# Kernel tuning notes

Measured on AMD Instinct MI355X. Metric: run time of the kernel, lower is better.

The kernel has to match this reference:

```python
import jax, jax.numpy as jnp
import numpy as np

N_NODES, N_EDGES, N_FEAT = 50000, 500000, 128
HID, LAT, N_GRAPHS = 256, 64, 512
HEADS, DH = 8, 32  # GAT: 8 heads x 32 = 256
EPS = 1e-5


def _seg_softmax(logits, seg, num):
    m = jax.ops.segment_max(logits, seg, num_segments=num)
    m = jnp.where(jnp.isfinite(m), m, 0.0)
    e = jnp.exp(logits - m[seg])
    s = jax.ops.segment_sum(e, seg, num_segments=num)
    return e / jnp.maximum(s[seg], 1e-16)


def _bn(h, g, b):  # BatchNorm1d, batch statistics
    mu = h.mean(0)
    var = h.var(0)
    return (h - mu) * jax.lax.rsqrt(var + EPS) * g + b


def _ln(h, g, b):
    mu = h.mean(-1, keepdims=True)
    var = h.var(-1, keepdims=True)
    return (h - mu) * jax.lax.rsqrt(var + EPS) * g + b


def setup_inputs() -> dict:
    key = jax.random.key(0)
    ks = iter(jax.random.split(key, 40))
    f = lambda *s: jax.random.normal(next(ks), s, dtype=jnp.float32) * 0.05
    inp = {
        'x': jax.random.normal(next(ks), (N_NODES, N_FEAT), dtype=jnp.float32),
        'W_emb': f(N_FEAT, HID), 'b_emb': f(HID),
        'W_gcn': f(HID, HID), 'b_gcn': f(HID),
        'W_gat': f(HID, HID), 'a_src': f(HEADS, DH), 'a_dst': f(HEADS, DH), 'b_gat': f(HID),
        'W_l': f(HID, HID), 'b_l': f(HID), 'W_r': f(HID, HID),
        'bn_gamma': jnp.ones((3, HID), jnp.float32), 'bn_beta': jnp.zeros((3, HID), jnp.float32),
        'Wg1': f(HID, HID // 2), 'bg1': f(HID // 2), 'Wg2': f(HID // 2, 1), 'bg2': f(1),
        'Wm1': f(HID, HID), 'bm1': f(HID), 'ln_m_g': jnp.ones(HID, jnp.float32), 'ln_m_b': jnp.zeros(HID, jnp.float32),
        'Wm2': f(HID, LAT), 'bm2': f(LAT),
        'Wv1': f(HID, HID), 'bv1': f(HID), 'ln_v_g': jnp.ones(HID, jnp.float32), 'ln_v_b': jnp.zeros(HID, jnp.float32),
        'Wv2': f(HID, LAT), 'bv2': f(LAT),
        'edge_index': jax.random.randint(next(ks), (2, N_EDGES), 0, N_NODES, dtype=jnp.int64),
        'batch': jnp.sort(jax.random.randint(next(ks), (N_NODES,), 0, N_GRAPHS, dtype=jnp.int64)),
    }
    return inp


def _forward(x, W_emb, b_emb, W_gcn, b_gcn, W_gat, a_src, a_dst, b_gat,
             W_l, b_l, W_r, bn_gamma, bn_beta, Wg1, bg1, Wg2, bg2,
             Wm1, bm1, ln_m_g, ln_m_b, Wm2, bm2, Wv1, bv1, ln_v_g, ln_v_b, Wv2, bv2,
             edge_index, batch):
    N = x.shape[0]
    loops = jnp.arange(N)
    src_sl = jnp.concatenate([edge_index[0], loops])  # with self-loops (GCN/GAT)
    dst_sl = jnp.concatenate([edge_index[1], loops])

    h = x @ W_emb + b_emb  # [N, HID]

    # --- layer 0: GCNConv ---
    deg = jax.ops.segment_sum(jnp.ones_like(dst_sl, dtype=h.dtype), dst_sl, num_segments=N)
    dis = jax.lax.rsqrt(deg)
    norm = dis[src_sl] * dis[dst_sl]  # [E+N]
    xt = h @ W_gcn
    out = jax.ops.segment_sum(xt[src_sl] * norm[:, None], dst_sl, num_segments=N) + b_gcn
    out = jax.nn.relu(_bn(out, bn_gamma[0], bn_beta[0]))
    h = h + out

    # --- layer 1: GATConv (8 heads, concat) ---
    xt = (h @ W_gat).reshape(N, HEADS, DH)
    al_src = (xt * a_src).sum(-1)  # [N, H]
    al_dst = (xt * a_dst).sum(-1)
    logits = jax.nn.leaky_relu(al_src[src_sl] + al_dst[dst_sl], 0.2)  # [E+N, H]
    alpha = _seg_softmax(logits, dst_sl, N)
    out = jax.ops.segment_sum(xt[src_sl] * alpha[:, :, None], dst_sl, num_segments=N)
    out = out.reshape(N, HID) + b_gat
    out = jax.nn.relu(_bn(out, bn_gamma[1], bn_beta[1]))
    h = h + out

    # --- layer 2: SAGEConv (mean aggregation, no self-loops) ---
    src, dst = edge_index[0], edge_index[1]
    cnt = jax.ops.segment_sum(jnp.ones_like(dst, dtype=h.dtype), dst, num_segments=N)
    nb_mean = jax.ops.segment_sum(h[src], dst, num_segments=N) / jnp.maximum(cnt, 1.0)[:, None]
    out = nb_mean @ W_l + b_l + h @ W_r
    out = jax.nn.relu(_bn(out, bn_gamma[2], bn_beta[2]))
    h = h + out

    # --- GlobalAttention pooling ---
    gate = (jax.nn.relu(h @ Wg1 + bg1) @ Wg2 + bg2)[:, 0]  # [N]
    w = _seg_softmax(gate, batch, N_GRAPHS)
    h_graph = jax.ops.segment_sum(h * w[:, None], batch, num_segments=N_GRAPHS)  # [G, HID]

    mu = jax.nn.relu(_ln(h_graph @ Wm1 + bm1, ln_m_g, ln_m_b)) @ Wm2 + bm2
    logvar = jax.nn.relu(_ln(h_graph @ Wv1 + bv1, ln_v_g, ln_v_b)) @ Wv2 + bv2
    return mu, logvar


def reference(x, W_emb, b_emb, W_gcn, b_gcn, W_gat, a_src, a_dst, b_gat,
              W_l, b_l, W_r, bn_gamma, bn_beta, Wg1, bg1, Wg2, bg2,
              Wm1, bm1, ln_m_g, ln_m_b, Wm2, bm2, Wv1, bv1, ln_v_g, ln_v_b, Wv2, bv2,
              edge_index, batch):
    return _forward(x, W_emb, b_emb, W_gcn, b_gcn, W_gat, a_src, a_dst, b_gat,
                    W_l, b_l, W_r, bn_gamma, bn_beta, Wg1, bg1, Wg2, bg2,
                    Wm1, bm1, ln_m_g, ln_m_b, Wm2, bm2, Wv1, bv1, ln_v_g, ln_v_b, Wv2, bv2,
                    edge_index, batch)
```

## Files before the change

### kernel.cpp

```cpp
#include <hip/hip_runtime.h>
#include <cstdint>
#include <cstddef>

#define N_NODES 50000
#define N_EDGES 500000
#define NG 512
#define HID 256
#define EPS 1e-5f
#define SCB 49

typedef __attribute__((ext_vector_type(8))) __bf16 bf16x8;
typedef __attribute__((ext_vector_type(8))) ushort u16x8;
typedef __attribute__((ext_vector_type(4))) float f32x4;

__device__ __forceinline__ ushort f2bf(float f) {
  uint32_t u = __float_as_uint(f);
  uint32_t r = (u + 0x7fffu + ((u >> 16) & 1u)) >> 16;
  return (ushort)r;
}
__device__ __forceinline__ float bfu(ushort u) { return __uint_as_float(((uint32_t)u) << 16); }
__device__ __forceinline__ float4 bf4(ushort4 u) {
  return make_float4(bfu(u.x), bfu(u.y), bfu(u.z), bfu(u.w));
}

__global__ void k_csr_count(const int* __restrict__ ei, int* __restrict__ cnt) {
  int e = blockIdx.x * 256 + threadIdx.x;
  if (e < N_EDGES) atomicAdd(&cnt[ei[N_EDGES + e]], 1);
}

__global__ void k_scan_part(const int* __restrict__ cnt, int* __restrict__ psum) {
  __shared__ int red[256];
  int tid = threadIdx.x;
  int i0 = blockIdx.x * 1024 + tid * 4;
  int s = 0;
  if (i0 + 4 <= N_NODES) {
    int4 v = *reinterpret_cast<const int4*>(cnt + i0);
    s = v.x + v.y + v.z + v.w;
  } else {
    for (int k = 0; k < 4; k++)
      if (i0 + k < N_NODES) s += cnt[i0 + k];
  }
  red[tid] = s;
  __syncthreads();
  for (int o = 128; o > 0; o >>= 1) {
    if (tid < o) red[tid] += red[tid + o];
    __syncthreads();
  }
  if (tid == 0) psum[blockIdx.x] = red[0];
}

__global__ void k_scan_top(const int* __restrict__ psum, int* __restrict__ boff,
                           int* __restrict__ row_ptr) {
  int t = threadIdx.x;
  int v = (t < SCB) ? psum[t] : 0;
  int own = v;
  for (int o = 1; o < 64; o <<= 1) {
    int u = __shfl_up(v, o);
    if (t >= o) v += u;
  }
  if (t < SCB) boff[t] = v - own;
  if (t == 63) row_ptr[N_NODES] = v;
}

__global__ void k_scan_out(const int* __restrict__ cnt, const int* __restrict__ boff,
                           int* __restrict__ row_ptr, float* __restrict__ dis) {
  __shared__ int ps[256];
  int tid = threadIdx.x;
  int i0 = blockIdx.x * 1024 + tid * 4;
  int v[4];
#pragma unroll
  for (int k = 0; k < 4; k++) v[k] = (i0 + k < N_NODES) ? cnt[i0 + k] : 0;
  int s = v[0] + v[1] + v[2] + v[3];
  ps[tid] = s;
  __syncthreads();
  for (int o = 1; o < 256; o <<= 1) {
    int add = (tid >= o) ? ps[tid - o] : 0;
    __syncthreads();
    ps[tid] += add;
    __syncthreads();
  }
  int run = boff[blockIdx.x] + ((tid > 0) ? ps[tid - 1] : 0);
#pragma unroll
  for (int k = 0; k < 4; k++) {
    if (i0 + k < N_NODES) {
      row_ptr[i0 + k] = run;
      dis[i0 + k] = rsqrtf((float)v[k] + 1.0f);
      run += v[k];
    }
  }
}

__global__ void k_csr_fill(const int* __restrict__ ei, const int* __restrict__ row_ptr,
                           int* __restrict__ fill, int* __restrict__ col_src) {
  int e = blockIdx.x * 256 + threadIdx.x;
  if (e >= N_EDGES) return;
  int s = ei[e], d = ei[N_EDGES + e];
  int pos = row_ptr[d] + atomicAdd(&fill[d], 1);
  col_src[pos] = s;
}

struct WtArgs {
  const float* src[6];
  ushort* dst[6];
  int K[6];
  int C[6];
  int off[6];
};

__global__ void k_wt_all(WtArgs a) {
  int b = blockIdx.x;
  int ji = 0;
#pragma unroll
  for (int t = 1; t < 6; t++)
    if (b >= a.off[t]) ji = t;
  int K = a.K[ji], C = a.C[ji];
  int i = (b - a.off[ji]) * 256 + threadIdx.x;
  int c = i / K, k = i - c * K;
  a.dst[ji][i] = f2bf(a.src[ji][k * C + c]);
}

template <int K, int C, bool DUAL, bool AFP32, bool GATE, bool GATAL, bool BNF>
__global__ __launch_bounds__(256) void k_mgemm(
    const void* __restrict__ A1v, const ushort* __restrict__ W1t,
    const ushort* __restrict__ A2, const ushort* __restrict__ W2t,
    const float* __restrict__ bias, ushort* __restrict__ out_bf,
    const float* __restrict__ gw, const float* __restrict__ gb,
    float* __restrict__ gate, const float* __restrict__ asv,
    const float* __restrict__ adv, float* __restrict__ als,
    float* __restrict__ ald, const float* __restrict__ scsh,
    ushort* __restrict__ hbuf, int M, int relu) {
  constexpr int KS = K / 32;
  constexpr int KSH = KS / 2;
  constexpr int KHALF = K / 2;
  constexpr int CHKH = KHALF / 8;
  constexpr int NPAN = C / 64;
  constexpr int LOWB = DUAL ? 4 : 2;
  constexpr int NTOT = NPAN * LOWB;
  constexpr int NISS = (64 * CHKH) / 256;
  constexpr int PELEM = 64 * KHALF;
  __shared__ ushort wlds[2 * PELEM];
  const int tid = threadIdx.x;
  const int lane = tid & 63;
  const int wid = tid >> 6;
  const int r16 = lane & 15;
  const int kg = lane >> 4;
  const int rbase = blockIdx.x * 64 + wid * 16;

  const bool avalid = (rbase + r16) < M;
  int arow = rbase + r16;
  if (arow >= M) arow = M - 1;

  bf16x8 af[KS], af2[KS];
  if constexpr (BNF) {
    const ushort* xp = (const ushort*)A1v + (size_t)arow * K + kg * 8;
    ushort* hp = hbuf + (size_t)arow * K + kg * 8;
#pragma unroll
    for (int ks = 0; ks < KS; ks++) {
      int col = kg * 8 + ks * 32;
      u16x8 xv = *reinterpret_cast<const u16x8*>(xp + ks * 32);
      u16x8 hv = *reinterpret_cast<const u16x8*>(hp + ks * 32);
      float4 sc0 = *reinterpret_cast<const float4*>(scsh + col);
      float4 sc1 = *reinterpret_cast<const float4*>(scsh + col + 4);
      float4 sh0 = *reinterpret_cast<const float4*>(scsh + 256 + col);
      float4 sh1 = *reinterpret_cast<const float4*>(scsh + 256 + col + 4);
      float scv[8] = {sc0.x, sc0.y, sc0.z, sc0.w, sc1.x, sc1.y, sc1.z, sc1.w};
      float shv[8] = {sh0.x, sh0.y, sh0.z, sh0.w, sh1.x, sh1.y, sh1.z, sh1.w};
      union { u16x8 u; bf16x8 b; } cv;
#pragma unroll
      for (int j = 0; j < 8; j++) {
        float v = fmaf(bfu(xv[j]), scv[j], shv[j]);
        float hn = bfu(hv[j]) + fmaxf(v, 0.f);
        cv.u[j] = f2bf(hn);
      }
      af[ks] = cv.b;
      if (avalid) *reinterpret_cast<u16x8*>(hp + ks * 32) = cv.u;
    }
  } else if constexpr (AFP32) {
    const float* ap = (const float*)A1v + (size_t)arow * K + kg * 8;
#pragma unroll
    for (int ks = 0; ks < KS; ks++) {
      float4 lo = *reinterpret_cast<const float4*>(ap + ks * 32);
      float4 hi = *reinterpret_cast<const float4*>(ap + ks * 32 + 4);
      union { u16x8 u; bf16x8 b; } cv;
      cv.u = (u16x8){f2bf(lo.x), f2bf(lo.y), f2bf(lo.z), f2bf(lo.w),
                     f2bf(hi.x), f2bf(hi.y), f2bf(hi.z), f2bf(hi.w)};
      af[ks] = cv.b;
    }
  } else {
    const ushort* ap = (const ushort*)A1v + (size_t)arow * K + kg * 8;
#pragma unroll
    for (int ks = 0; ks < KS; ks++)
      af[ks] = *reinterpret_cast<const bf16x8*>(ap + ks * 32);
  }
  if constexpr (DUAL) {
    const ushort* ap = A2 + (size_t)arow * K + kg * 8;
#pragma unroll
    for (int ks = 0; ks < KS; ks++)
      af2[ks] = *reinterpret_cast<const bf16x8*>(ap + ks * 32);
  }

  float greg[4] = {0.f, 0.f, 0.f, 0.f};
  f32x4 acc[4];

#define STAGE_ASYNC(WSRC, PAN, KH, BUF)                                        \
  {                                                                            \
    const ushort* base_ = (WSRC) + (size_t)((PAN) * 64) * K + (KH) * KHALF;    \
    _Pragma("unroll") for (int j = 0; j < NISS; j++) {                         \
      int p_ = j * 256 + tid;                                                  \
      int c_ = p_ / CHKH, jj_ = p_ % CHKH;                                     \
      const ushort* g_ = base_ + c_ * K + (jj_ ^ (c_ & 7)) * 8;                \
      ushort* l_ = &wlds[(BUF) * PELEM + (j * 256 + wid * 64) * 8];            \
      __builtin_amdgcn_global_load_lds(                                        \
          (const __attribute__((address_space(1))) void*)(g_),                 \
          (__attribute__((address_space(3))) void*)(l_), 16, 0, 0);            \
    }                                                                          \
  }

#define COMPUTE(AF, KH, BUF)                                                   \
  {                                                                            \
    const ushort* wb_ = &wlds[(BUF) * PELEM];                                  \
    _Pragma("unroll") for (int ct = 0; ct < 4; ct++) {                         \
      bf16x8 wf[KSH];                                                          \
      int colr = ct * 16 + r16;                                                \
      _Pragma("unroll") for (int ksl = 0; ksl < KSH; ksl++) {                  \
        int slot = colr * CHKH + ((ksl * 4 + kg) ^ (r16 & 7));                 \
        wf[ksl] = *reinterpret_cast<const bf16x8*>(&wb_[slot * 8]);            \
      }                                                                        \
      _Pragma("unroll") for (int ksl = 0; ksl < KSH; ksl++)                    \
        acc[ct] = __builtin_amdgcn_mfma_f32_16x16x32_bf16(                     \
            (AF)[(KH) * KSH + ksl], wf[ksl], acc[ct], 0, 0, 0);                \
    }                                                                          \
  }

  STAGE_ASYNC(W1t, 0, 0, 0);
  __syncthreads();

#pragma unroll
  for (int q = 0; q < NTOT; q++) {
    const int kh = q & 1;
    const int pass = DUAL ? ((q >> 1) & 1) : 0;
    const int pan = DUAL ? (q >> 2) : (q >> 1);
    const int cur = q & 1 ? 1 : 0;
    const int bufq = q & 1;
    const int c0 = pan * 64;
    if ((q & (LOWB - 1)) == 0) {
#pragma unroll
      for (int ct = 0; ct < 4; ct++) acc[ct] = (f32x4){0.f, 0.f, 0.f, 0.f};
    }
    if (q + 1 < NTOT) {
      const int nkh = (q + 1) & 1;
      const int npass = DUAL ? (((q + 1) >> 1) & 1) : 0;
      const int npan = DUAL ? ((q + 1) >> 2) : ((q + 1) >> 1);
      const ushort* Wq = (DUAL && npass) ? W2t : W1t;
      STAGE_ASYNC(Wq, npan, nkh, bufq ^ 1);
    }
    if (DUAL && pass) {
      COMPUTE(af2, kh, bufq);
    } else {
      COMPUTE(af, kh, bufq);
    }
    if ((q & (LOWB - 1)) == (LOWB - 1)) {
      if constexpr (GATE) {
#pragma unroll
        for (int ct = 0; ct < 4; ct++) {
          int col = c0 + ct * 16 + r16;
          float bv = bias[col];
          float wv = gw[col];
#pragma unroll
          for (int i = 0; i < 4; i++) {
            float v = fmaxf(acc[ct][i] + bv, 0.f);
            greg[i] = fmaf(v, wv, greg[i]);
          }
        }
      } else {
#pragma unroll
        for (int ct = 0; ct < 4; ct++) {
          int col = c0 + ct * 16 + r16;
          float bv = bias ? bias[col] : 0.f;
#pragma unroll
          for (int i = 0; i < 4; i++) {
            int row = rbase + kg * 4 + i;
            if (row < M) {
              float v = acc[ct][i] + bv;
              if (relu) v = fmaxf(v, 0.f);
              out_bf[(size_t)row * C + col] = f2bf(v);
            }
          }
        }
      }
      if constexpr (GATAL) {
        float ps_[2][4], pd_[2][4];
#pragma unroll
        for (int h2 = 0; h2 < 2; h2++)
#pragma unroll
          for (int i = 0; i < 4; i++) { ps_[h2][i] = 0.f; pd_[h2][i] = 0.f; }
#pragma unroll
        for (int ct = 0; ct < 4; ct++) {
          int col = c0 + ct * 16 + r16;
          float as_ = asv[col], ad_ = adv[col];
          int h2 = ct >> 1;
#pragma unroll
          for (int i = 0; i < 4; i++) {
            ps_[h2][i] = fmaf(acc[ct][i], as_, ps_[h2][i]);
            pd_[h2][i] = fmaf(acc[ct][i], ad_, pd_[h2][i]);
          }
        }
#pragma unroll
        for (int h2 = 0; h2 < 2; h2++)
#pragma unroll
          for (int i = 0; i < 4; i++) {
#pragma unroll
            for (int o = 1; o < 16; o <<= 1) {
              ps_[h2][i] += __shfl_xor(ps_[h2][i], o);
              pd_[h2][i] += __shfl_xor(pd_[h2][i], o);
            }
          }
        if (r16 == 0) {
#pragma unroll
          for (int h2 = 0; h2 < 2; h2++) {
            int head = pan * 2 + h2;
#pragma unroll
            for (int i = 0; i < 4; i++) {
              int row = rbase + kg * 4 + i;
              if (row < M) {
                als[(size_t)head * N_NODES + row] = ps_[h2][i];
                ald[(size_t)head * N_NODES + row] = pd_[h2][i];
              }
            }
          }
        }
      }
    }
    __syncthreads();
  }

  if constexpr (GATE) {
#pragma unroll
    for (int i = 0; i < 4; i++) {
#pragma unroll
      for (int o = 1; o < 16; o <<= 1) greg[i] += __shfl_xor(greg[i], o);
    }
    if (r16 == 0) {
      float b0 = gb[0];
#pragma unroll
      for (int i = 0; i < 4; i++) {
        int row = rbase + kg * 4 + i;
        if (row < M) gate[row] = greg[i] + b0;
      }
    }
  }
#undef STAGE_ASYNC
#undef COMPUTE
}

__global__ void k_gcn_agg(const ushort* __restrict__ xt, const float* __restrict__ dis,
                          const int* __restrict__ row_ptr, const int* __restrict__ col_src,
                          const float* __restrict__ b_gcn, ushort* __restrict__ outb) {
  int node = blockIdx.x * 4 + (threadIdx.x >> 6);
  if (node >= N_NODES) return;
  int lane = threadIdx.x & 63;
  int half = lane >> 5;
  int c0 = (lane & 31) * 8;
  float di = dis[node];
  float acc[8];
#pragma unroll
  for (int j = 0; j < 8; j++) acc[j] = 0.f;
  int b = row_ptr[node], e = row_ptr[node + 1];
  int g0 = b;
  for (; g0 + 8 <= e; g0 += 8) {
    int i0 = g0 + half * 4;
    int s0 = col_src[i0], s1 = col_src[i0 + 1], s2 = col_src[i0 + 2], s3 = col_src[i0 + 3];
    float w0 = di * dis[s0], w1 = di * dis[s1], w2 = di * dis[s2], w3 = di * dis[s3];
    u16x8 u0 = *reinterpret_cast<const u16x8*>(xt + (size_t)s0 * HID + c0);
    u16x8 u1 = *reinterpret_cast<const u16x8*>(xt + (size_t)s1 * HID + c0);
    u16x8 u2 = *reinterpret_cast<const u16x8*>(xt + (size_t)s2 * HID + c0);
    u16x8 u3 = *reinterpret_cast<const u16x8*>(xt + (size_t)s3 * HID + c0);
#pragma unroll
    for (int j = 0; j < 8; j++) {
      acc[j] = fmaf(bfu(u0[j]), w0, acc[j]);
      acc[j] = fmaf(bfu(u1[j]), w1, acc[j]);
      acc[j] = fmaf(bfu(u2[j]), w2, acc[j]);
      acc[j] = fmaf(bfu(u3[j]), w3, acc[j]);
    }
  }
  for (; g0 + 4 <= e; g0 += 4) {
    int i0 = g0 + half * 2;
    int s0 = col_src[i0], s1 = col_src[i0 + 1];
    float w0 = di * dis[s0], w1 = di * dis[s1];
    u16x8 u0 = *reinterpret_cast<const u16x8*>(xt + (size_t)s0 * HID + c0);
    u16x8 u1 = *reinterpret_cast<const u16x8*>(xt + (size_t)s1 * HID + c0);
#pragma unroll
    for (int j = 0; j < 8; j++) {
      acc[j] = fmaf(bfu(u0[j]), w0, acc[j]);
      acc[j] = fmaf(bfu(u1[j]), w1, acc[j]);
    }
  }
  {
    int i0 = g0 + half * 2;
    int s0 = 0, s1 = 0;
    float w0 = 0.f, w1 = 0.f;
    if (i0 < e) { s0 = col_src[i0]; w0 = di * dis[s0]; }
    if (i0 + 1 < e) { s1 = col_src[i0 + 1]; w1 = di * dis[s1]; }
    u16x8 u0 = *reinterpret_cast<const u16x8*>(xt + (size_t)s0 * HID + c0);
    u16x8 u1 = *reinterpret_cast<const u16x8*>(xt + (size_t)s1 * HID + c0);
#pragma unroll
    for (int j = 0; j < 8; j++) {
      acc[j] = fmaf(bfu(u0[j]), w0, acc[j]);
      acc[j] = fmaf(bfu(u1[j]), w1, acc[j]);
    }
  }
#pragma unroll
  for (int j = 0; j < 8; j++) acc[j] += __shfl_xor(acc[j], 32);
  if (!half) {
    u16x8 un = *reinterpret_cast<const u16x8*>(xt + (size_t)node * HID + c0);
    float w0 = di * di;
    u16x8 r;
#pragma unroll
    for (int j = 0; j < 8; j++) {
      float v = fmaf(bfu(un[j]), w0, acc[j]) + b_gcn[c0 + j];
      r[j] = f2bf(v);
    }
    *reinterpret_cast<u16x8*>(outb + (size_t)node * HID + c0) = r;
  }
}

__device__ __forceinline__ float leaky02(float x) { return x > 0.f ? x : 0.2f * x; }

__global__ void k_gat_agg(const ushort* __restrict__ xt, const float* __restrict__ alsrc,
                          const float* __restrict__ aldst, const int* __restrict__ row_ptr,
                          const int* __restrict__ col_src, const float* __restrict__ b_gat,
                          ushort* __restrict__ outb) {
  int node = blockIdx.x * 4 + (threadIdx.x >> 6);
  if (node >= N_NODES) return;
  int lane = threadIdx.x & 63;
  int half = lane >> 5;
  int l32 = lane & 31;
  int c0 = l32 * 8;
  int hh = l32 >> 2;
  const float* alh = alsrc + (size_t)hh * N_NODES;
  float ad = aldst[(size_t)hh * N_NODES + node];
  float acc[8];
#pragma unroll
  for (int j = 0; j < 8; j++) acc[j] = 0.f;
  float s = 0.f;
  int b = row_ptr[node], e = row_ptr[node + 1];
  int g0 = b;
  for (; g0 + 8 <= e; g0 += 8) {
    int i0 = g0 + half * 4;
    int s0 = col_src[i0], s1 = col_src[i0 + 1], s2 = col_src[i0 + 2], s3 = col_src[i0 + 3];
    float g0v = alh[s0], g1v = alh[s1], g2v = alh[s2], g3v = alh[s3];
    u16x8 u0 = *reinterpret_cast<const u16x8*>(xt + (size_t)s0 * HID + c0);
    u16x8 u1 = *reinterpret_cast<const u16x8*>(xt + (size_t)s1 * HID + c0);
    u16x8 u2 = *reinterpret_cast<const u16x8*>(xt + (size_t)s2 * HID + c0);
    u16x8 u3 = *reinterpret_cast<const u16x8*>(xt + (size_t)s3 * HID + c0);
    float a0 = __expf(leaky02(g0v + ad));
    float a1 = __expf(leaky02(g1v + ad));
    float a2 = __expf(leaky02(g2v + ad));
    float a3 = __expf(leaky02(g3v + ad));
    s += a0 + a1 + a2 + a3;
#pragma unroll
    for (int j = 0; j < 8; j++) {
      acc[j] = fmaf(bfu(u0[j]), a0, acc[j]);
      acc[j] = fmaf(bfu(u1[j]), a1, acc[j]);
      acc[j] = fmaf(bfu(u2[j]), a2, acc[j]);
      acc[j] = fmaf(bfu(u3[j]), a3, acc[j]);
    }
  }
  for (; g0 + 4 <= e; g0 += 4) {
    int i0 = g0 + half * 2;
    int s0 = col_src[i0], s1 = col_src[i0 + 1];
    float a0 = __expf(leaky02(alh[s0] + ad));
    float a1 = __expf(leaky02(alh[s1] + ad));
    u16x8 u0 = *reinterpret_cast<const u16x8*>(xt + (size_t)s0 * HID + c0);
    u16x8 u1 = *reinterpret_cast<const u16x8*>(xt + (size_t)s1 * HID + c0);
    s += a0 + a1;
#pragma unroll
    for (int j = 0; j < 8; j++) {
      acc[j] = fmaf(bfu(u0[j]), a0, acc[j]);
      acc[j] = fmaf(bfu(u1[j]), a1, acc[j]);
    }
  }
  {
    int i0 = g0 + half * 2;
    int s0 = 0, s1 = 0;
    float a0 = 0.f, a1 = 0.f;
    if (i0 < e) { s0 = col_src[i0]; a0 = __expf(leaky02(alh[s0] + ad)); }
    if (i0 + 1 < e) { s1 = col_src[i0 + 1]; a1 = __expf(leaky02(alh[s1] + ad)); }
    u16x8 u0 = *reinterpret_cast<const u16x8*>(xt + (size_t)s0 * HID + c0);
    u16x8 u1 = *reinterpret_cast<const u16x8*>(xt + (size_t)s1 * HID + c0);
    s += a0 + a1;
#pragma unroll
    for (int j = 0; j < 8; j++) {
      acc[j] = fmaf(bfu(u0[j]), a0, acc[j]);
      acc[j] = fmaf(bfu(u1[j]), a1, acc[j]);
    }
  }
#pragma unroll
  for (int j = 0; j < 8; j++) acc[j] += __shfl_xor(acc[j], 32);
  s += __shfl_xor(s, 32);
  if (!half) {
    float e0 = __expf(leaky02(alh[node] + ad));
    u16x8 un = *reinterpret_cast<const u16x8*>(xt + (size_t)node * HID + c0);
    float inv_s = 1.0f / (s + e0);
    u16x8 r;
#pragma unroll
    for (int j = 0; j < 8; j++) {
      float v = fmaf(bfu(un[j]), e0, acc[j]) * inv_s + b_gat[c0 + j];
      r[j] = f2bf(v);
    }
    *reinterpret_cast<u16x8*>(outb + (size_t)node * HID + c0) = r;
  }
}

__global__ void k_sage_agg(const ushort* __restrict__ h, const int* __restrict__ row_ptr,
                           const int* __restrict__ col_src, ushort* __restrict__ outb) {
  int node = blockIdx.x * 4 + (threadIdx.x >> 6);
  if (node >= N_NODES) return;
  int lane = threadIdx.x & 63;
  int half = lane >> 5;
  int c0 = (lane & 31) * 8;
  float acc[8];
#pragma unroll
  for (int j = 0; j < 8; j++) acc[j] = 0.f;
  int b = row_ptr[node], e = row_ptr[node + 1];
  int g0 = b;
  for (; g0 + 8 <= e; g0 += 8) {
    int i0 = g0 + half * 4;
    int s0 = col_src[i0], s1 = col_src[i0 + 1], s2 = col_src[i0 + 2], s3 = col_src[i0 + 3];
    u16x8 u0 = *reinterpret_cast<const u16x8*>(h + (size_t)s0 * HID + c0);
    u16x8 u1 = *reinterpret_cast<const u16x8*>(h + (size_t)s1 * HID + c0);
    u16x8 u2 = *reinterpret_cast<const u16x8*>(h + (size_t)s2 * HID + c0);
    u16x8 u3 = *reinterpret_cast<const u16x8*>(h + (size_t)s3 * HID + c0);
#pragma unroll
    for (int j = 0; j < 8; j++)
      acc[j] += (bfu(u0[j]) + bfu(u1[j])) + (bfu(u2[j]) + bfu(u3[j]));
  }
  for (; g0 + 4 <= e; g0 += 4) {
    int i0 = g0 + half * 2;
    int s0 = col_src[i0], s1 = col_src[i0 + 1];
    u16x8 u0 = *reinterpret_cast<const u16x8*>(h + (size_t)s0 * HID + c0);
    u16x8 u1 = *reinterpret_cast<const u16x8*>(h + (size_t)s1 * HID + c0);
#pragma unroll
    for (int j = 0; j < 8; j++) acc[j] += bfu(u0[j]) + bfu(u1[j]);
  }
  {
    int i0 = g0 + half * 2;
    int s0 = 0, s1 = 0;
    float w0 = 0.f, w1 = 0.f;
    if (i0 < e) { s0 = col_src[i0]; w0 = 1.f; }
    if (i0 + 1 < e) { s1 = col_src[i0 + 1]; w1 = 1.f; }
    u16x8 u0 = *reinterpret_cast<const u16x8*>(h + (size_t)s0 * HID + c0);
    u16x8 u1 = *reinterpret_cast<const u16x8*>(h + (size_t)s1 * HID + c0);
#pragma unroll
    for (int j = 0; j < 8; j++) {
      acc[j] = fmaf(bfu(u0[j]), w0, acc[j]);
      acc[j] = fmaf(bfu(u1[j]), w1, acc[j]);
    }
  }
#pragma unroll
  for (int j = 0; j < 8; j++) acc[j] += __shfl_xor(acc[j], 32);
  if (!half) {
    float inv = 1.0f / fmaxf((float)(e - b), 1.0f);
    u16x8 r;
#pragma unroll
    for (int j = 0; j < 8; j++) r[j] = f2bf(acc[j] * inv);
    *reinterpret_cast<u16x8*>(outb + (size_t)node * HID + c0) = r;
  }
}

__global__ __launch_bounds__(256) void k_bn_stats(const ushort* __restrict__ x,
                                                  float* __restrict__ stats) {
  int tid = threadIdx.x;
  int cg = tid & 31;
  int rs = tid >> 5;
  int c0 = cg * 8;
  float s[8], q[8];
#pragma unroll
  for (int j = 0; j < 8; j++) { s[j] = 0.f; q[j] = 0.f; }
  for (int r = blockIdx.x * 8 + rs; r < N_NODES; r += gridDim.x * 8) {
    u16x8 v = *reinterpret_cast<const u16x8*>(x + (size_t)r * HID + c0);
#pragma unroll
    for (int j = 0; j < 8; j++) {
      float f = bfu(v[j]);
      s[j] += f;
      q[j] = fmaf(f, f, q[j]);
    }
  }
  __shared__ float ls[512];
  ls[tid] = 0.f;
  ls[tid + 256] = 0.f;
  __syncthreads();
#pragma unroll
  for (int j = 0; j < 8; j++) {
    atomicAdd(&ls[c0 + j], s[j]);
    atomicAdd(&ls[256 + c0 + j], q[j]);
  }
  __syncthreads();
  atomicAdd(&stats[tid], ls[tid]);
  atomicAdd(&stats[tid + 256], ls[tid + 256]);
}

__global__ void k_bn_coef(const float* __restrict__ stats, const float* __restrict__ gamma,
                          const float* __restrict__ beta, float* __restrict__ scsh) {
  int c = threadIdx.x;
  const float invN = 1.0f / (float)N_NODES;
  float mu = stats[c] * invN;
  float var = stats[256 + c] * invN - mu * mu;
  float sc = gamma[c] * rsqrtf(var + EPS);
  scsh[c] = sc;
  scsh[256 + c] = beta[c] - mu * sc;
}

__global__ void k_bn_apply(const ushort* __restrict__ x, const float* __restrict__ scsh,
                           ushort* __restrict__ h_bf) {
  int total = N_NODES * 64;
  for (int i = blockIdx.x * 256 + threadIdx.x; i < total; i += gridDim.x * 256) {
    int c4 = (i & 63) * 4;
    float4 xv = bf4(*reinterpret_cast<const ushort4*>(x + (size_t)i * 4));
    float4 sc = *reinterpret_cast<const float4*>(scsh + c4);
    float4 sh = *reinterpret_cast<const float4*>(scsh + 256 + c4);
    float4 hv = bf4(*reinterpret_cast<const ushort4*>(h_bf + (size_t)i * 4));
    hv.x += fmaxf(fmaf(xv.x, sc.x, sh.x), 0.f);
    hv.y += fmaxf(fmaf(xv.y, sc.y, sh.y), 0.f);
    hv.z += fmaxf(fmaf(xv.z, sc.z, sh.z), 0.f);
    hv.w += fmaxf(fmaf(xv.w, sc.w, sh.w), 0.f);
    *reinterpret_cast<ushort4*>(h_bf + (size_t)i * 4) =
        make_ushort4(f2bf(hv.x), f2bf(hv.y), f2bf(hv.z), f2bf(hv.w));
  }
}

__global__ void k_gstart(const int* __restrict__ batch, int* __restrict__ gstart) {
  int g = blockIdx.x * 256 + threadIdx.x;
  if (g > NG) return;
  int lo = 0, hi = N_NODES;
  while (lo < hi) {
    int mid = (lo + hi) >> 1;
    if (batch[mid] < g) lo = mid + 1; else hi = mid;
  }
  gstart[g] = lo;
}

__global__ void k_pool(const ushort* __restrict__ hb, const float* __restrict__ gate,
                       const int* __restrict__ gstart, float* __restrict__ hg) {
  __shared__ float red[256];
  __shared__ float wbuf[256];
  int g = blockIdx.x, tid = threadIdx.x;
  int b = gstart[g], e = gstart[g + 1];
  float m = -1e30f;
  for (int r = b + tid; r < e; r += 256) m = fmaxf(m, gate[r]);
  red[tid] = m;
  __syncthreads();
  for (int o = 128; o > 0; o >>= 1) {
    if (tid < o) red[tid] = fmaxf(red[tid], red[tid + o]);
    __syncthreads();
  }
  m = red[0];
  __syncthreads();
  float s = 0.f;
  for (int r = b + tid; r < e; r += 256) s += __expf(gate[r] - m);
  red[tid] = s;
  __syncthreads();
  for (int o = 128; o > 0; o >>= 1) {
    if (tid < o) red[tid] += red[tid + o];
    __syncthreads();
  }
  float inv = 1.0f / fmaxf(red[0], 1e-16f);
  __syncthreads();
  float acc = 0.f;
  for (int cb = b; cb < e; cb += 256) {
    int r = cb + tid;
    wbuf[tid] = (r < e) ? __expf(gate[r] - m) : 0.f;
    __syncthreads();
    int n = min(256, e - cb);
    for (int j = 0; j < n; j++)
      acc = fmaf(bfu(hb[(size_t)(cb + j) * HID + tid]), wbuf[j], acc);
    __syncthreads();
  }
  hg[(size_t)g * HID + tid] = acc * inv;
}

__global__ void k_mlp(const float* __restrict__ hg, const float* __restrict__ W1,
                      const float* __restrict__ b1, const float* __restrict__ lng,
                      const float* __restrict__ lnb, const float* __restrict__ W2,
                      const float* __restrict__ b2, float* __restrict__ out) {
  __shared__ float row[HID];
  __shared__ float z[HID];
  __shared__ float red[HID];
  int g = blockIdx.x, tid = threadIdx.x;
  row[tid] = hg[(size_t)g * HID + tid];
  __syncthreads();
  float acc = b1[tid];
  for (int k = 0; k < HID; k++) acc = fmaf(row[k], W1[(size_t)k * HID + tid], acc);
  red[tid] = acc;
  __syncthreads();
  for (int o = 128; o > 0; o >>= 1) {
    if (tid < o) red[tid] += red[tid + o];
    __syncthreads();
  }
  float mu = red[0] * (1.0f / HID);
  __syncthreads();
  red[tid] = acc * acc;
  __syncthreads();
  for (int o = 128; o > 0; o >>= 1) {
    if (tid < o) red[tid] += red[tid + o];
    __syncthreads();
  }
  float var = red[0] * (1.0f / HID) - mu * mu;
  float zz = (acc - mu) * rsqrtf(var + EPS) * lng[tid] + lnb[tid];
  z[tid] = fmaxf(zz, 0.f);
  __syncthreads();
  if (tid < 64) {
    float o = b2[tid];
    for (int k = 0; k < HID; k++) o = fmaf(z[k], W2[(size_t)k * 64 + tid], o);
    out[(size_t)g * 64 + tid] = o;
  }
}

extern "C" void kernel_launch(void* const* d_in, const int* in_sizes, int n_in,
                              void* d_out, int out_size, void* d_ws, size_t ws_size,
                              hipStream_t stream) {
  const float* x     = (const float*)d_in[0];
  const float* W_emb = (const float*)d_in[1];
  const float* b_emb = (const float*)d_in[2];
  const float* W_gcn = (const float*)d_in[3];
  const float* b_gcn = (const float*)d_in[4];
  const float* W_gat = (const float*)d_in[5];
  const float* a_src = (const float*)d_in[6];
  const float* a_dst = (const float*)d_in[7];
  const float* b_gat = (const float*)d_in[8];
  const float* W_l   = (const float*)d_in[9];
  const float* b_l   = (const float*)d_in[10];
  const float* W_r   = (const float*)d_in[11];
  const float* bn_g  = (const float*)d_in[12];
  const float* bn_b  = (const float*)d_in[13];
  const float* Wg1   = (const float*)d_in[14];
  const float* bg1   = (const float*)d_in[15];
  const float* Wg2   = (const float*)d_in[16];
  const float* bg2   = (const float*)d_in[17];
  const float* Wm1   = (const float*)d_in[18];
  const float* bm1   = (const float*)d_in[19];
  const float* lnmg  = (const float*)d_in[20];
  const float* lnmb  = (const float*)d_in[21];
  const float* Wm2   = (const float*)d_in[22];
  const float* bm2   = (const float*)d_in[23];
  const float* Wv1   = (const float*)d_in[24];
  const float* bv1   = (const float*)d_in[25];
  const float* lnvg  = (const float*)d_in[26];
  const float* lnvb  = (const float*)d_in[27];
  const float* Wv2   = (const float*)d_in[28];
  const float* bv2   = (const float*)d_in[29];
  const int* ei      = (const int*)d_in[30];
  const int* batch   = (const int*)d_in[31];
  float* out = (float*)d_out;

  float* ws = (float*)d_ws;
  float* h     = ws;
  float* t1    = h + (size_t)N_NODES * HID;
  float* alsrc = t1 + (size_t)N_NODES * HID;
  float* aldst = alsrc + N_NODES * 8;
  float* dis   = aldst + N_NODES * 8;
  float* gate  = dis + N_NODES;
  float* hg    = gate + N_NODES;
  float* zbase = hg + NG * HID;
  float* bnst  = zbase;
  int* row_cnt = (int*)(zbase + 3 * 512);
  int* fill    = row_cnt + N_NODES;
  int* row_ptr = fill + N_NODES;
  int* col_src = row_ptr + N_NODES + 1;
  int* gstart  = col_src + N_EDGES;
  int* psum    = gstart + NG + 1;
  int* boff    = psum + 64;
  float* scsh  = (float*)(boff + 64);

  ushort* t1b = (ushort*)t1;

  size_t off = (size_t)((char*)(scsh + 3 * 512) - (char*)d_ws);
  off = (off + 15) & ~(size_t)15;
  ushort* h_bf   = (ushort*)((char*)d_ws + off);
  ushort* t0_bf  = h_bf + (size_t)N_NODES * HID;
  ushort* wemb_t = t0_bf + (size_t)N_NODES * HID;
  ushort* wgcn_t = wemb_t + 128 * 256;
  ushort* wgat_t = wgcn_t + 256 * 256;
  ushort* wr_t   = wgat_t + 256 * 256;
  ushort* wl_t   = wr_t + 256 * 256;
  ushort* wg1_t  = wl_t + 256 * 256;

  size_t zbytes = (size_t)3 * 512 * 4 + 2 * (size_t)N_NODES * 4;
  hipMemsetAsync(zbase, 0, zbytes, stream);

  k_csr_count<<<(N_EDGES + 255) / 256, 256, 0, stream>>>(ei, row_cnt);
  k_scan_part<<<SCB, 256, 0, stream>>>(row_cnt, psum);
  k_scan_top<<<1, 64, 0, stream>>>(psum, boff, row_ptr);
  k_scan_out<<<SCB, 256, 0, stream>>>(row_cnt, boff, row_ptr, dis);
  k_csr_fill<<<(N_EDGES + 255) / 256, 256, 0, stream>>>(ei, row_ptr, fill, col_src);

  WtArgs wa;
  wa.src[0] = W_emb; wa.dst[0] = wemb_t; wa.K[0] = 128; wa.C[0] = 256; wa.off[0] = 0;
  wa.src[1] = W_gcn; wa.dst[1] = wgcn_t; wa.K[1] = 256; wa.C[1] = 256; wa.off[1] = 128;
  wa.src[2] = W_gat; wa.dst[2] = wgat_t; wa.K[2] = 256; wa.C[2] = 256; wa.off[2] = 384;
  wa.src[3] = W_r;   wa.dst[3] = wr_t;   wa.K[3] = 256; wa.C[3] = 256; wa.off[3] = 640;
  wa.src[4] = W_l;   wa.dst[4] = wl_t;   wa.K[4] = 256; wa.C[4] = 256; wa.off[4] = 896;
  wa.src[5] = Wg1;   wa.dst[5] = wg1_t;  wa.K[5] = 256; wa.C[5] = 128; wa.off[5] = 1152;
  k_wt_all<<<1280, 256, 0, stream>>>(wa);

  const int RB = (N_NODES + 63) / 64;
  const int AB = (N_NODES + 3) / 4;

  k_mgemm<128, 256, false, true, false, false, false><<<RB, 256, 0, stream>>>(
      x, wemb_t, nullptr, nullptr, b_emb, h_bf, nullptr, nullptr, nullptr,
      nullptr, nullptr, nullptr, nullptr, nullptr, nullptr, N_NODES, 0);

  k_mgemm<256, 256, false, false, false, false, false><<<RB, 256, 0, stream>>>(
      h_bf, wgcn_t, nullptr, nullptr, nullptr, t0_bf, nullptr, nullptr, nullptr,
      nullptr, nullptr, nullptr, nullptr, nullptr, nullptr, N_NODES, 0);
  k_gcn_agg<<<AB, 256, 0, stream>>>(t0_bf, dis, row_ptr, col_src, b_gcn, t1b);
  k_bn_stats<<<1024, 256, 0, stream>>>(t1b, bnst);
  k_bn_coef<<<1, 256, 0, stream>>>(bnst, bn_g, bn_b, scsh);

  k_mgemm<256, 256, false, false, false, true, true><<<RB, 256, 0, stream>>>(
      t1b, wgat_t, nullptr, nullptr, nullptr, t0_bf, nullptr, nullptr, nullptr,
      a_src, a_dst, alsrc, aldst, scsh, h_bf, N_NODES, 0);
  k_gat_agg<<<AB, 256, 0, stream>>>(t0_bf, alsrc, aldst, row_ptr, col_src, b_gat, t1b);
  k_bn_stats<<<1024, 256, 0, stream>>>(t1b, bnst + 512);
  k_bn_coef<<<1, 256, 0, stream>>>(bnst + 512, bn_g + HID, bn_b + HID, scsh + 512);
  k_bn_apply<<<1024, 256, 0, stream>>>(t1b, scsh + 512, h_bf);

  k_sage_agg<<<AB, 256, 0, stream>>>(h_bf, row_ptr, col_src, t0_bf);
  k_mgemm<256, 256, true, false, false, false, false><<<RB, 256, 0, stream>>>(
      h_bf, wr_t, t0_bf, wl_t, b_l, t1b, nullptr, nullptr, nullptr,
      nullptr, nullptr, nullptr, nullptr, nullptr, nullptr, N_NODES, 0);
  k_bn_stats<<<1024, 256, 0, stream>>>(t1b, bnst + 1024);
  k_bn_coef<<<1, 256, 0, stream>>>(bnst + 1024, bn_g + 2 * HID, bn_b + 2 * HID, scsh + 1024);

  k_mgemm<256, 128, false, false, true, false, true><<<RB, 256, 0, stream>>>(
      t1b, wg1_t, nullptr, nullptr, bg1, nullptr, Wg2, bg2, gate,
      nullptr, nullptr, nullptr, nullptr, scsh + 1024, h_bf, N_NODES, 1);
  k_gstart<<<3, 256, 0, stream>>>(batch, gstart);
  k_pool<<<NG, 256, 0, stream>>>(h_bf, gate, gstart, hg);

  k_mlp<<<NG, 256, 0, stream>>>(hg, Wm1, bm1, lnmg, lnmb, Wm2, bm2, out);
  k_mlp<<<NG, 256, 0, stream>>>(hg, Wv1, bv1, lnvg, lnvb, Wv2, bv2, out + (size_t)NG * 64);
}
```

Before: 550.6 us.

## Fold embedding into GCN weight and interleave GAT attention logits per node

Precomputes W_emb@W_gcn and b_emb@W_gcn in a small kernel, so the GCN linear transform runs as a K=128 GEMM straight from fp32 x instead of a K=256 GEMM over the bf16 embedding. It also changes the GAT source/destination attention scalars from head-major to node-major [N,8] layout, so the per-edge gathers for the 8 heads of one source node fall in the same cache line. The fold rounds the combined weight to bf16, which slightly changes numerics, and the embedding GEMM still runs because its output is used for the residual.

Measured after the change: 564.3 us. 2.5% more time.

```diff
diff --git a/kernel.cpp b/kernel.cpp
--- a/kernel.cpp
+++ b/kernel.cpp
@@ -117,6 +117,23 @@
   int i = (b - a.off[ji]) * 256 + threadIdx.x;
   int c = i / K, k = i - c * K;
   a.dst[ji][i] = f2bf(a.src[ji][k * C + c]);
+}
+
+__global__ void k_wfold(const float* __restrict__ We, const ushort* __restrict__ Wg_t,
+                        ushort* __restrict__ Wc_t, float* __restrict__ bc,
+                        const float* __restrict__ b_emb, const float* __restrict__ W_gcn) {
+  int c = blockIdx.x;
+  int k = threadIdx.x;
+  const float* wr = We + k * 256;
+  const ushort* gr = Wg_t + c * 256;
+  float s = 0.f;
+  for (int j = 0; j < 256; j++) s = fmaf(wr[j], bfu(gr[j]), s);
+  Wc_t[c * 128 + k] = f2bf(s);
+  if (k == 0) {
+    float t = 0.f;
+    for (int j = 0; j < 256; j++) t = fmaf(b_emb[j], W_gcn[j * 256 + c], t);
+    bc[c] = t;
+  }
 }
 
 template <int K, int C, bool DUAL, bool AFP32, bool GATE, bool GATAL, bool BNF>
@@ -240,7 +257,6 @@
     const int kh = q & 1;
     const int pass = DUAL ? ((q >> 1) & 1) : 0;
     const int pan = DUAL ? (q >> 2) : (q >> 1);
-    const int cur = q & 1 ? 1 : 0;
     const int bufq = q & 1;
     const int c0 = pan * 64;
     if ((q & (LOWB - 1)) == 0) {
@@ -317,15 +333,13 @@
           }
         if (r16 == 0) {
 #pragma unroll
-          for (int h2 = 0; h2 < 2; h2++) {
-            int head = pan * 2 + h2;
-#pragma unroll
-            for (int i = 0; i < 4; i++) {
-              int row = rbase + kg * 4 + i;
-              if (row < M) {
-                als[(size_t)head * N_NODES + row] = ps_[h2][i];
-                ald[(size_t)head * N_NODES + row] = pd_[h2][i];
-              }
+          for (int i = 0; i < 4; i++) {
+            int row = rbase + kg * 4 + i;
+            if (row < M) {
+              als[row * 8 + pan * 2 + 0] = ps_[0][i];
+              ald[row * 8 + pan * 2 + 0] = pd_[0][i];
+              als[row * 8 + pan * 2 + 1] = ps_[1][i];
+              ald[row * 8 + pan * 2 + 1] = pd_[1][i];
             }
           }
         }
@@ -437,8 +451,7 @@
   int l32 = lane & 31;
   int c0 = l32 * 8;
   int hh = l32 >> 2;
-  const float* alh = alsrc + (size_t)hh * N_NODES;
-  float ad = aldst[(size_t)hh * N_NODES + node];
+  float ad = aldst[node * 8 + hh];
   float acc[8];
 #pragma unroll
   for (int j = 0; j < 8; j++) acc[j] = 0.f;
@@ -448,7 +461,8 @@
   for (; g0 + 8 <= e; g0 += 8) {
     int i0 = g0 + half * 4;
     int s0 = col_src[i0], s1 = col_src[i0 + 1], s2 = col_src[i0 + 2], s3 = col_src[i0 + 3];
-    float g0v = alh[s0], g1v = alh[s1], g2v = alh[s2], g3v = alh[s3];
+    float g0v = alsrc[s0 * 8 + hh], g1v = alsrc[s1 * 8 + hh];
+    float g2v = alsrc[s2 * 8 + hh], g3v = alsrc[s3 * 8 + hh];
     u16x8 u0 = *reinterpret_cast<const u16x8*>(xt + (size_t)s0 * HID + c0);
     u16x8 u1 = *reinterpret_cast<const u16x8*>(xt + (size_t)s1 * HID + c0);
     u16x8 u2 = *reinterpret_cast<const u16x8*>(xt + (size_t)s2 * HID + c0);
@@ -469,8 +483,8 @@
   for (; g0 + 4 <= e; g0 += 4) {
     int i0 = g0 + half * 2;
     int s0 = col_src[i0], s1 = col_src[i0 + 1];
-    float a0 = __expf(leaky02(alh[s0] + ad));
-    float a1 = __expf(leaky02(alh[s1] + ad));
+    float a0 = __expf(leaky02(alsrc[s0 * 8 + hh] + ad));
+    float a1 = __expf(leaky02(alsrc[s1 * 8 + hh] + ad));
     u16x8 u0 = *reinterpret_cast<const u16x8*>(xt + (size_t)s0 * HID + c0);
     u16x8 u1 = *reinterpret_cast<const u16x8*>(xt + (size_t)s1 * HID + c0);
     s += a0 + a1;
@@ -484,8 +498,8 @@
     int i0 = g0 + half * 2;
     int s0 = 0, s1 = 0;
     float a0 = 0.f, a1 = 0.f;
-    if (i0 < e) { s0 = col_src[i0]; a0 = __expf(leaky02(alh[s0] + ad)); }
-    if (i0 + 1 < e) { s1 = col_src[i0 + 1]; a1 = __expf(leaky02(alh[s1] + ad)); }
+    if (i0 < e) { s0 = col_src[i0]; a0 = __expf(leaky02(alsrc[s0 * 8 + hh] + ad)); }
+    if (i0 + 1 < e) { s1 = col_src[i0 + 1]; a1 = __expf(leaky02(alsrc[s1 * 8 + hh] + ad)); }
     u16x8 u0 = *reinterpret_cast<const u16x8*>(xt + (size_t)s0 * HID + c0);
     u16x8 u1 = *reinterpret_cast<const u16x8*>(xt + (size_t)s1 * HID + c0);
     s += a0 + a1;
@@ -499,7 +513,7 @@
   for (int j = 0; j < 8; j++) acc[j] += __shfl_xor(acc[j], 32);
   s += __shfl_xor(s, 32);
   if (!half) {
-    float e0 = __expf(leaky02(alh[node] + ad));
+    float e0 = __expf(leaky02(alsrc[node * 8 + hh] + ad));
     u16x8 un = *reinterpret_cast<const u16x8*>(xt + (size_t)node * HID + c0);
     float inv_s = 1.0f / (s + e0);
     u16x8 r;
@@ -771,10 +785,11 @@
   int* psum    = gstart + NG + 1;
   int* boff    = psum + 64;
   float* scsh  = (float*)(boff + 64);
+  float* bc    = scsh + 3 * 512;
 
   ushort* t1b = (ushort*)t1;
 
-  size_t off = (size_t)((char*)(scsh + 3 * 512) - (char*)d_ws);
+  size_t off = (size_t)((char*)(bc + 256) - (char*)d_ws);
   off = (off + 15) & ~(size_t)15;
   ushort* h_bf   = (ushort*)((char*)d_ws + off);
   ushort* t0_bf  = h_bf + (size_t)N_NODES * HID;
@@ -784,6 +799,7 @@
   ushort* wr_t   = wgat_t + 256 * 256;
   ushort* wl_t   = wr_t + 256 * 256;
   ushort* wg1_t  = wl_t + 256 * 256;
+  ushort* wc_t   = wg1_t + 256 * 128;
 
   size_t zbytes = (size_t)3 * 512 * 4 + 2 * (size_t)N_NODES * 4;
   hipMemsetAsync(zbase, 0, zbytes, stream);
@@ -803,6 +819,8 @@
   wa.src[5] = Wg1;   wa.dst[5] = wg1_t;  wa.K[5] = 256; wa.C[5] = 128; wa.off[5] = 1152;
   k_wt_all<<<1280, 256, 0, stream>>>(wa);
 
+  k_wfold<<<256, 128, 0, stream>>>(W_emb, wgcn_t, wc_t, bc, b_emb, W_gcn);
+
   const int RB = (N_NODES + 63) / 64;
   const int AB = (N_NODES + 3) / 4;
 
@@ -810,8 +828,8 @@
       x, wemb_t, nullptr, nullptr, b_emb, h_bf, nullptr, nullptr, nullptr,
       nullptr, nullptr, nullptr, nullptr, nullptr, nullptr, N_NODES, 0);
 
-  k_mgemm<256, 256, false, false, false, false, false><<<RB, 256, 0, stream>>>(
-      h_bf, wgcn_t, nullptr, nullptr, nullptr, t0_bf, nullptr, nullptr, nullptr,
+  k_mgemm<128, 256, false, true, false, false, false><<<RB, 256, 0, stream>>>(
+      x, wc_t, nullptr, nullptr, bc, t0_bf, nullptr, nullptr, nullptr,
       nullptr, nullptr, nullptr, nullptr, nullptr, nullptr, N_NODES, 0);
   k_gcn_agg<<<AB, 256, 0, stream>>>(t0_bf, dis, row_ptr, col_src, b_gcn, t1b);
   k_bn_stats<<<1024, 256, 0, stream>>>(t1b, bnst);
```
